# Performance work log

Hardware: AMD Instinct MI355X
Metric: run time of the kernel (lower is better)

Reference implementation:

```python
import jax, jax.numpy as jnp
import numpy as np

EPS = 1e-5
BN_GAMMA = 1.0
BN_BETA = 1e-4  # per torch init: BN weight=1, bias=0.0001


def bn(h):
    # BatchNorm1d in training mode: biased batch variance
    mu = h.mean(axis=0)
    var = h.var(axis=0)
    return (h - mu) * (BN_GAMMA / jnp.sqrt(var + EPS)) + BN_BETA


def gcn_conv(h, W, b, row, col, n, edge_weight=None):
    # PyG-style GCNConv: linear -> add self loops (w=1) -> sym deg norm -> scatter-sum
    h = h @ W
    e = row.shape[0]
    ew = jnp.ones((e,), h.dtype) if edge_weight is None else edge_weight
    loop = jnp.arange(n, dtype=row.dtype)
    r = jnp.concatenate([row, loop])
    c = jnp.concatenate([col, loop])
    w = jnp.concatenate([ew, jnp.ones((n,), h.dtype)])
    deg = jax.ops.segment_sum(w, r, num_segments=n)
    dinv = jnp.where(deg > 0, jax.lax.rsqrt(deg + jnp.where(deg > 0, 0.0, 1.0)), 0.0)
    norm = dinv[r] * w * dinv[c]  # [E+N]
    msg = h[r] * norm[:, None]    # gather + per-edge scale
    out = jax.ops.segment_sum(msg, c, num_segments=n)  # scatter-aggregate
    return out + b


def readout(h, W1, b1, W2, b2):
    h = bn(h) @ W1 + b1
    h = bn(jax.nn.relu(h)) @ W2 + b2
    return jax.nn.log_softmax(h, axis=-1)


def setup_inputs() -> dict:
    key = jax.random.key(0)
    ks = jax.random.split(key, 12)
    N, E, F, H, C = 50000, 800000, 128, 128, 10
    s = 0.05
    return {
        "x": jax.random.normal(ks[0], (N, F), jnp.float32),
        "edge_index": jax.random.randint(ks[1], (2, E), 0, N, jnp.int32),
        "perm": jax.random.permutation(ks[2], N).astype(jnp.int32),
        "W_feat": jax.random.normal(ks[3], (F, H), jnp.float32) * s,
        "b_feat": jnp.zeros((H,), jnp.float32),
        "W_convs": jax.random.normal(ks[4], (3, H, H), jnp.float32) * s,
        "b_convs": jnp.zeros((3, H), jnp.float32),
        "W_ea": jax.random.normal(ks[5], (2 * H, 2), jnp.float32) * s,
        "b_ea": jnp.zeros((2,), jnp.float32),
        "W_na": jax.random.normal(ks[6], (H, 2), jnp.float32) * s,
        "b_na": jnp.zeros((2,), jnp.float32),
        "W_ctx": jax.random.normal(ks[7], (H, H), jnp.float32) * s,
        "b_ctx": jnp.zeros((H,), jnp.float32),
        "W_obj": jax.random.normal(ks[8], (H, H), jnp.float32) * s,
        "b_obj": jnp.zeros((H,), jnp.float32),
        "W_fc1": jax.random.normal(ks[9], (3, H, H), jnp.float32) * s,  # c,o,co
        "b_fc1": jnp.zeros((3, H), jnp.float32),
        "W_fc2": jax.random.normal(ks[10], (3, H, C), jnp.float32) * s,
        "b_fc2": jnp.zeros((3, C), jnp.float32),
    }


def reference(x, edge_index, perm, W_feat, b_feat, W_convs, b_convs, W_ea, b_ea,
              W_na, b_na, W_ctx, b_ctx, W_obj, b_obj, W_fc1, b_fc1, W_fc2, b_fc2):
    n = x.shape[0]
    row, col = edge_index[0], edge_index[1]
    h = bn(x)
    h = jax.nn.relu(h @ W_feat + b_feat)  # conv_feat has gfn=True -> pure linear
    for i in range(3):
        h = jax.nn.relu(gcn_conv(bn(h), W_convs[i], b_convs[i], row, col, n))
    edge_rep = jnp.concatenate([h[row], h[col]], axis=-1)  # [E, 2H]
    edge_att = jax.nn.softmax(edge_rep @ W_ea + b_ea, axis=-1)
    node_att = jax.nn.softmax(h @ W_na + b_na, axis=-1)
    xc = node_att[:, 0:1] * h
    xo = node_att[:, 1:2] * h
    xc = jax.nn.relu(gcn_conv(bn(xc), W_ctx, b_ctx, row, col, n, edge_att[:, 0]))
    xo = jax.nn.relu(gcn_conv(bn(xo), W_obj, b_obj, row, col, n, edge_att[:, 1]))
    xc_logis = readout(xc, W_fc1[0], b_fc1[0], W_fc2[0], b_fc2[0])
    xo_logis = readout(xo, W_fc1[1], b_fc1[1], W_fc2[1], b_fc2[1])
    xco_logis = readout(xc[perm] + xo, W_fc1[2], b_fc1[2], W_fc2[2], b_fc2[2])
    return (xc_logis, xo_logis, xco_logis)
```

## Files before the change

kernel.cpp:

```cpp
#include <hip/hip_runtime.h>
#include <math.h>

#define H 128
#define NCLS 10
#define EPS 1e-5f
#define BN_BETA 1e-4f
#define CS_BLOCKS 256

typedef unsigned short u16;
typedef unsigned int u32;
typedef __attribute__((ext_vector_type(8))) short short8;
typedef __attribute__((ext_vector_type(4))) float floatx4;

__device__ inline float bflo(u32 u) { union { u32 i; float f; } a; a.i = u << 16; return a.f; }
__device__ inline float bfhi(u32 u) { union { u32 i; float f; } a; a.i = u & 0xffff0000u; return a.f; }
__device__ inline u16 f2bf(float f) {
  union { float f; u32 i; } v; v.f = f;
  return (u16)((v.i + 0x7fff + ((v.i >> 16) & 1)) >> 16);
}
__device__ inline u32 pack2(float a, float b) { return (u32)f2bf(a) | ((u32)f2bf(b) << 16); }

__device__ inline void reduce_partials(const float* __restrict__ P, int nb, int stride,
                                       int off0, int f, float* su_out, float* sq_out) {
  float su[8] = {0, 0, 0, 0, 0, 0, 0, 0}, sq[8] = {0, 0, 0, 0, 0, 0, 0, 0};
// ... 9 lines not shown
  for (; b < nb; b++) {
    const float* p = P + (size_t)b * stride + off0;
    su[0] += p[f];
    sq[0] += p[128 + f];
  }
  *su_out = ((su[0] + su[1]) + (su[2] + su[3])) + ((su[4] + su[5]) + (su[6] + su[7]));
  *sq_out = ((sq[0] + sq[1]) + (sq[2] + sq[3])) + ((sq[4] + sq[5]) + (sq[6] + sq[7]));
}

__device__ inline void fold256_body(const float* P, int nb, int stride, int off0,
                                    const float* W, const float* bias, float invN,
                                    int kp, u16* Wt, float* cf) {
  int f = threadIdx.x & 127;
  int half = threadIdx.x >> 7;
  int k = kp * 2 + half;
  float su, sq;
  reduce_partials(P, nb, stride, off0, f, &su, &sq);
  float mu = su * invN;
  float var = sq * invN - mu * mu;
  float s = 1.0f / sqrtf(fmaxf(var, 0.f) + EPS);
  float w = W[(size_t)f * H + k];
  Wt[(size_t)k * H + f] = f2bf(s * w);
  __shared__ float red[2][128];
  red[half][f] = (BN_BETA - mu * s) * w;
  __syncthreads();
  for (int o = 64; o > 0; o >>= 1) {
    if (f < o) red[half][f] += red[half][f + o];
    __syncthreads();
  }
  if (f == 0) cf[k] = red[half][0] + (bias ? bias[k] : 0.f);
}

__device__ inline void hist_body(const int* __restrict__ row, const int* __restrict__ col,
                                 int E, int* cnt, float* deg, int blk) {
  int e = blk * 256 + threadIdx.x;
  if (e < E) {
    atomicAdd(&cnt[col[e]], 1);
    atomicAdd(&deg[row[e]], 1.0f);
  }
}

__device__ inline void xstats_body(const float* __restrict__ x, int n4,
                                   float* __restrict__ stp, int blk) {
  int tid = threadIdx.x;
  int lane = tid & 63, wave = tid >> 6;
  float s[4] = {0, 0, 0, 0}, q[4] = {0, 0, 0, 0};
  int step = CS_BLOCKS * 256;
  for (int i = blk * 256 + tid; i < n4; i += step) {
    float4 v = ((const float4*)x)[i];
    s[0] += v.x; q[0] += v.x * v.x; s[1] += v.y; q[1] += v.y * v.y;
    s[2] += v.z; q[2] += v.z * v.z; s[3] += v.w; q[3] += v.w * v.w;
  }
#pragma unroll
  for (int k = 0; k < 4; k++) { s[k] += __shfl_xor(s[k], 32); q[k] += __shfl_xor(q[k], 32); }
  __shared__ float smx[4][256];
  int col = (lane & 31) * 4;
  if (lane < 32) {
#pragma unroll
    for (int k = 0; k < 4; k++) { smx[wave][col + k] = s[k]; smx[wave][128 + col + k] = q[k]; }
  }
  __syncthreads();
  stp[(size_t)blk * 256 + tid] = smx[0][tid] + smx[1][tid] + smx[2][tid] + smx[3][tid];
}

__device__ inline void scanA_body(const int* cnt, const float* deg, int N,
                                  int* partial, float* dinv, float* degc, int blk) {
  int i = blk * 256 + threadIdx.x;
  if (i < N) {
    dinv[i] = 1.0f / sqrtf(deg[i] + 1.0f);
    degc[i] = 0.f;
  }
  __shared__ int sdA[256];
  sdA[threadIdx.x] = (i < N) ? cnt[i] : 0;
  __syncthreads();
  for (int o = 128; o > 0; o >>= 1) {
    if (threadIdx.x < o) sdA[threadIdx.x] += sdA[threadIdx.x + o];
    __syncthreads();
  }
  if (threadIdx.x == 0) partial[blk] = sdA[0];
}

__device__ inline void scanB_body(const int* partial, int nb, int* blockoff) {
  __shared__ int sdB[256];
  int t = threadIdx.x;
  int v = (t < nb) ? partial[t] : 0;
  sdB[t] = v;
  __syncthreads();
  for (int o = 1; o < 256; o <<= 1) {
    int x = (t >= o) ? sdB[t - o] : 0;
    __syncthreads();
    sdB[t] += x;
    __syncthreads();
  }
  blockoff[t] = sdB[t] - v;
}

__device__ inline void scanC_body(const int* cnt, int N, const int* blockoff,
                                  int* off, int* cur, int E, int blk) {
  __shared__ int sdC[256];
  int t = threadIdx.x;
  int i = blk * 256 + t;
  int v = (i < N) ? cnt[i] : 0;
  sdC[t] = v;
  __syncthreads();
  for (int o = 1; o < 256; o <<= 1) {
    int x = (t >= o) ? sdC[t - o] : 0;
    __syncthreads();
    sdC[t] += x;
    __syncthreads();
  }
  if (i < N) {
    int ex = blockoff[blk] + sdC[t] - v;
    off[i] = ex;
    cur[i] = ex;
  }
  if (i == 0) off[N] = E;
}

__device__ inline void place_body(const int* row, const int* col, int E, int* cur,
                                  const float* dinv, int* csr_src, int* slot_of,
                                  float* wn, int blk) {
  int e = blk * 256 + threadIdx.x;
  if (e < E) {
    int r = row[e];
    int slot = atomicAdd(&cur[col[e]], 1);
    csr_src[slot] = r;
    slot_of[e] = slot;
    wn[slot] = dinv[r];
  }
}

__device__ inline void eatt_body(const int* row, const int* col, int E,
                                 const float2* p01, const float2* q01,
                                 const float* b_ea, const int* slot_of,
                                 float* att0s, float* degc, int blk) {
  int e = blk * 256 + threadIdx.x;
  if (e >= E) return;
  int r = row[e], c = col[e];
  float2 p = p01[r], q = q01[c];
  float l0 = p.x + q.x + b_ea[0];
  float l1 = p.y + q.y + b_ea[1];
  float a0 = 1.0f / (1.0f + expf(l1 - l0));
  att0s[slot_of[e]] = a0;
  atomicAdd(&degc[r], a0);
}

__device__ inline void xprestats_body(const u16* __restrict__ h,
                                      const float2* __restrict__ na01, int n4,
                                      float* __restrict__ stp, int blk) {
  int tid = threadIdx.x;
  int lane = tid & 63, wave = tid >> 6;
  float sc[4] = {0, 0, 0, 0}, qc[4] = {0, 0, 0, 0};
  float so[4] = {0, 0, 0, 0}, qo[4] = {0, 0, 0, 0};
  int step = CS_BLOCKS * 256;
  for (int i = blk * 256 + tid; i < n4; i += step) {
    int n = i >> 5;
    uint2 u = ((const uint2*)h)[i];
    float v0 = bflo(u.x), v1 = bfhi(u.x), v2 = bflo(u.y), v3 = bfhi(u.y);
    float2 ab = na01[n];
    float a = ab.x, b = ab.y;
    float c0 = v0 * a, c1 = v1 * a, c2 = v2 * a, c3 = v3 * a;
    float o0 = v0 * b, o1 = v1 * b, o2 = v2 * b, o3 = v3 * b;
    sc[0] += c0; qc[0] += c0 * c0; sc[1] += c1; qc[1] += c1 * c1;
    sc[2] += c2; qc[2] += c2 * c2; sc[3] += c3; qc[3] += c3 * c3;
    so[0] += o0; qo[0] += o0 * o0; so[1] += o1; qo[1] += o1 * o1;
    so[2] += o2; qo[2] += o2 * o2; so[3] += o3; qo[3] += o3 * o3;
  }
#pragma unroll
  for (int k = 0; k < 4; k++) {
    sc[k] += __shfl_xor(sc[k], 32); qc[k] += __shfl_xor(qc[k], 32);
    so[k] += __shfl_xor(so[k], 32); qo[k] += __shfl_xor(qo[k], 32);
  }
  __shared__ float smp[4][512];
  int col = (lane & 31) * 4;
  if (lane < 32) {
#pragma unroll
    for (int k = 0; k < 4; k++) {
      smp[wave][col + k] = sc[k];
      smp[wave][128 + col + k] = qc[k];
      smp[wave][256 + col + k] = so[k];
      smp[wave][384 + col + k] = qo[k];
    }
  }
  __syncthreads();
  float r0 = smp[0][tid] + smp[1][tid] + smp[2][tid] + smp[3][tid];
  float r1 = smp[0][256 + tid] + smp[1][256 + tid] + smp[2][256 + tid] + smp[3][256 + tid];
  stp[(size_t)blk * 512 + tid] = r0;
  stp[(size_t)blk * 512 + 256 + tid] = r1;
}

__device__ inline void wa2_body(const int* csr_src, const float* att0s,
                                const float* deg, const float* degc,
                                const float2* na01, float2* wfa, float2* wfr,
                                int E, int blk) {
  int i = blk * 256 + threadIdx.x;
  if (i >= E) return;
  int s = csr_src[i];
  float a0 = att0s[i];
  float2 na = na01[s];
  float dgc = degc[s];
  float r0 = a0 / sqrtf(dgc + 1.0f);
  float r1 = (1.0f - a0) / sqrtf(deg[s] - dgc + 1.0f);
  wfa[i] = make_float2(r0 * na.x, r1 * na.y);
  wfr[i] = make_float2(r0, r1);
}

__device__ inline void gemm_core(const u16* A, const float* Afp, const u16* Bt,
                                 const float* cf, const float* b2, const float* sumw,
                                 u16* C, int N, int relu, int blk, float* stp) {
  int tid = threadIdx.x;
  int wave = tid >> 6, lane = tid & 63;
  int l15 = lane & 15, quad = lane >> 4;
  int row0 = (blk * 4 + wave) * 16;
  if (row0 >= N && !stp) return;
  int arow = row0 + l15;
  short8 a[4];
  short8 z8 = {0, 0, 0, 0, 0, 0, 0, 0};
  if (Afp) {
#pragma unroll
    for (int k4 = 0; k4 < 4; k4++) {
      if (arow < N) {
        const float* p = Afp + (size_t)arow * H + k4 * 32 + quad * 8;
        float4 f0 = *(const float4*)p;
        float4 f1 = *(const float4*)(p + 4);
        union { short8 s8; u32 u[4]; } cv;
        cv.u[0] = pack2(f0.x, f0.y); cv.u[1] = pack2(f0.z, f0.w);
        cv.u[2] = pack2(f1.x, f1.y); cv.u[3] = pack2(f1.z, f1.w);
        a[k4] = cv.s8;
      } else a[k4] = z8;
    }
  } else {
#pragma unroll
    for (int k4 = 0; k4 < 4; k4++)
      a[k4] = (arow < N) ? *(const short8*)(A + (size_t)arow * H + k4 * 32 + quad * 8) : z8;
  }
  float srow[4];
  if (sumw) {
#pragma unroll
    for (int r = 0; r < 4; r++) {
// ... 18 lines not shown
#pragma unroll
    for (int r = 0; r < 4; r++) {
      int row = row0 + quad * 4 + r;
      if (row < N) {
        float v = acc[r] + (sumw ? srow[r] * base + bb : base);
        if (relu) v = fmaxf(v, 0.f);
        s_ += v; q_ += v * v;
        C[(size_t)row * H + col] = f2bf(v);
      }
    }
    ps[nt] = s_; pq[nt] = q_;
  }
  if (stp) {
    __shared__ float sred[4][256];
#pragma unroll
    for (int nt = 0; nt < 8; nt++) {
      ps[nt] += __shfl_xor(ps[nt], 16); ps[nt] += __shfl_xor(ps[nt], 32);
      pq[nt] += __shfl_xor(pq[nt], 16); pq[nt] += __shfl_xor(pq[nt], 32);
    }
    if (quad == 0) {
#pragma unroll
      for (int nt = 0; nt < 8; nt++) {
        sred[wave][nt * 16 + l15] = ps[nt];
        sred[wave][128 + nt * 16 + l15] = pq[nt];
      }
    }
    __syncthreads();
    stp[(size_t)blk * 256 + tid] =
        sred[0][tid] + sred[1][tid] + sred[2][tid] + sred[3][tid];
  }
}

__global__ __launch_bounds__(256) void hist_xstats_kernel(
    const int* row, const int* col, int E, int* cnt, float* deg, int gE,
    const float* x, int n4, float* stpX) {
  if ((int)blockIdx.x < gE) hist_body(row, col, E, cnt, deg, blockIdx.x);
  else xstats_body(x, n4, stpX, blockIdx.x - gE);
}

__global__ __launch_bounds__(256) void scanA_fold_kernel(
    const int* cnt, const float* deg, int N, int* partial, float* dinv, float* degc,
    int SB, const float* stpX, const float* W_feat, const float* b_feat, float invN,
    u16* WtA, float* cfA) {
  if ((int)blockIdx.x < SB) scanA_body(cnt, deg, N, partial, dinv, degc, blockIdx.x);
  else fold256_body(stpX, CS_BLOCKS, 256, 0, W_feat, b_feat, invN, blockIdx.x - SB, WtA, cfA);
}

__global__ __launch_bounds__(256) void scanB_gemmx_kernel(
    const int* partial, int nb, int* blockoff,
    const float* x, const u16* WtA, const float* cfA, u16* C, int N, float* stpG) {
  if (blockIdx.x == 0) scanB_body(partial, nb, blockoff);
  else gemm_core(nullptr, x, WtA, cfA, nullptr, nullptr, C, N, 1, blockIdx.x - 1, stpG);
}

__global__ __launch_bounds__(256) void scanC_fold_kernel(
    const int* cnt, int N, const int* blockoff, int* off, int* cur, int E, int SB,
    const float* stpG, int nbG, const float* Wc, float invN, u16* WtB, float* cfB) {
  if ((int)blockIdx.x < SB) scanC_body(cnt, N, blockoff, off, cur, E, blockIdx.x);
  else fold256_body(stpG, nbG, 256, 0, Wc, nullptr, invN, blockIdx.x - SB, WtB, cfB);
}

__global__ __launch_bounds__(256) void place_gemm_kernel(
    const int* row, const int* col, int E, int* cur, const float* dinv,
    int* csr_src, int* slot_of, float* wn, int gE,
    const u16* A, const u16* WtB, const float* cfB, u16* C, int N) {
  if ((int)blockIdx.x < gE)
    place_body(row, col, E, cur, dinv, csr_src, slot_of, wn, blockIdx.x);
  else
    gemm_core(A, nullptr, WtB, cfB, nullptr, nullptr, C, N, 0, blockIdx.x - gE, nullptr);
}

__global__ __launch_bounds__(256) void eatt_xpre_kernel(
    const int* row, const int* col, int E, const float2* p01, const float2* q01,
    const float* b_ea, const int* slot_of, float* att0s, float* degc, int gE,
    const u16* h, const float2* na01, int n4, float* stpPre) {
  if ((int)blockIdx.x < gE)
    eatt_body(row, col, E, p01, q01, b_ea, slot_of, att0s, degc, blockIdx.x);
  else
    xprestats_body(h, na01, n4, stpPre, blockIdx.x - gE);
}

__global__ __launch_bounds__(256) void wa2_fold2_kernel(
    const int* csr_src, const float* att0s, const float* deg, const float* degc,
    const float2* na01, float2* wfa, float2* wfr, int E, int gE,
    const float* stpPre, const float* W_ctx, const float* W_obj, float invN,
    u16* Wt2, float* cf2) {
  if ((int)blockIdx.x < gE)
    wa2_body(csr_src, att0s, deg, degc, na01, wfa, wfr, E, blockIdx.x);
  else {
    int b = blockIdx.x - gE;
    int j = b >> 6, kp = b & 63;
    fold256_body(stpPre, CS_BLOCKS, 512, j * 256, j ? W_obj : W_ctx, nullptr, invN, kp,
                 Wt2 + (size_t)j * H * H, cf2 + j * H);
  }
}

__global__ __launch_bounds__(256) void fold256_kernel(
    const float* P, int nb, const float* W, const float* bias, float invN,
    u16* Wt, float* cf) {
  fold256_body(P, nb, 256, 0, W, bias, invN, blockIdx.x, Wt, cf);
}

__global__ __launch_bounds__(256) void fold3_kernel(
    const float* PC, int nbC, const float* PO, int nbO, const float* PCO, int nbCO,
    const float* W_fc1, const float* b_fc1, float invN, u16* Wt3, float* cf3) {
  int j = blockIdx.x / 64, kp = blockIdx.x % 64;
  const float* P = (j == 0) ? PC : (j == 1) ? PO : PCO;
  int nb = (j == 0) ? nbC : (j == 1) ? nbO : nbCO;
  fold256_body(P, nb, 256, 0, W_fc1 + (size_t)j * H * H, b_fc1 + j * H, invN, kp,
               Wt3 + (size_t)j * H * H, cf3 + j * H);
}

__global__ __launch_bounds__(128) void fold10x3_kernel(
    const float* stpZ, int nb, const float* W_fc2, const float* b_fc2, float invN,
    float* W2f, float* c2f) {
  int j = blockIdx.x / NCLS, k = blockIdx.x % NCLS;
  const float* P = stpZ + (size_t)j * nb * 256;
  int f = threadIdx.x;
  float su, sq;
  reduce_partials(P, nb, 256, 0, f, &su, &sq);
  float mu = su * invN;
  float var = sq * invN - mu * mu;
  float s = 1.0f / sqrtf(fmaxf(var, 0.f) + EPS);
  float w = W_fc2[(size_t)j * H * NCLS + (size_t)f * NCLS + k];
  W2f[(size_t)j * H * NCLS + (size_t)f * NCLS + k] = s * w;
  __shared__ float red1[H];
  red1[f] = (BN_BETA - mu * s) * w;
  __syncthreads();
  for (int o = 64; o > 0; o >>= 1) {
    if (f < o) red1[f] += red1[f + o];
    __syncthreads();
  }
  if (f == 0) c2f[j * 16 + k] = red1[0] + b_fc2[j * NCLS + k];
}

__global__ __launch_bounds__(256) void gemm_kernel(
    const u16* A, const u16* Bt, const float* cf, u16* C, int N, int relu) {
  gemm_core(A, nullptr, Bt, cf, nullptr, nullptr, C, N, relu, blockIdx.x, nullptr);
}

__global__ __launch_bounds__(256) void gemm2sw_kernel(
    u16* B0, u16* B1, const u16* Wt2, const float* cf2,
    const float* b0, const float* b1, const float* sw0, const float* sw1,
// ... 72 lines not shown
    int ix[8]; float wv[8];
#pragma unroll
    for (int u = 0; u < 8; u++) {
      int e = s + g + u * 4;
      bool ok = e < s1;
      int e2 = ok ? e : s0;
      ix[u] = csr_src[e2];
      wv[u] = ok ? wseg[e2] : 0.f;
    }
    uint4 uu[8];
#pragma unroll
    for (int u = 0; u < 8; u++) uu[u] = T[(size_t)ix[u] * 16 + li];
#pragma unroll
    for (int u = 0; u < 8; u++) { float w = wv[u] * dv; ACC8(acc, uu[u], w) }
  }
#pragma unroll
  for (int j = 0; j < 8; j++) {
    acc[j] += __shfl_xor(acc[j], 16);
    acc[j] += __shfl_xor(acc[j], 32);
  }
  if (g == 0) {
    float o[8];
#pragma unroll
    for (int j = 0; j < 8; j++) o[j] = fmaxf(acc[j] + bias[li * 8 + j], 0.f);
    uint4 w4;
    w4.x = pack2(o[0], o[1]); w4.y = pack2(o[2], o[3]);
    w4.z = pack2(o[4], o[5]); w4.w = pack2(o[6], o[7]);
    ((uint4*)out)[(size_t)v * 16 + li] = w4;
  }
}

__global__ __launch_bounds__(256) void aggdual_kernel(
    const u16* __restrict__ h, const int* __restrict__ csr_src,
    const float2* __restrict__ wfa, const float2* __restrict__ wfr,
    const int* __restrict__ off, const float* __restrict__ deg,
    const float* __restrict__ degc, const float2* __restrict__ na01,
    u16* __restrict__ gc, u16* __restrict__ go,
    float* __restrict__ sumw_c, float* __restrict__ sumw_o, int N) {
  int v = blockIdx.x * 4 + (threadIdx.x >> 6);
  if (v >= N) return;
  int lane = threadIdx.x & 63;
  int g = lane >> 4, li = lane & 15;
  const uint4* T = (const uint4*)h;
  float dgc = degc[v];
  float dvc = 1.0f / sqrtf(dgc + 1.0f);
  float dvo = 1.0f / sqrtf(deg[v] - dgc + 1.0f);
  float ac[8] = {0.f, 0.f, 0.f, 0.f, 0.f, 0.f, 0.f, 0.f};
  float ao[8] = {0.f, 0.f, 0.f, 0.f, 0.f, 0.f, 0.f, 0.f};
  float swc = 0.f, swo = 0.f;
  if (g == 0) {
    uint4 u = T[(size_t)v * 16 + li];
    float2 na = na01[v];
    float wc = dvc * dvc, wo = dvo * dvo;
    float wch = wc * na.x, woh = wo * na.y;
    ACC8(ac, u, wch)
    ACC8(ao, u, woh)
  }
  int s0 = off[v], s1 = off[v + 1];
  for (int s = s0; s < s1; s += 16) {
    int ix[4]; float2 fa[4], fr[4];
#pragma unroll
    for (int u = 0; u < 4; u++) {
      int e = s + g + u * 4;
      bool ok = e < s1;
      int e2 = ok ? e : s0;
      ix[u] = csr_src[e2];
      fa[u] = ok ? wfa[e2] : make_float2(0.f, 0.f);
      fr[u] = ok ? wfr[e2] : make_float2(0.f, 0.f);
    }
    uint4 uu[4];
#pragma unroll
    for (int u = 0; u < 4; u++) uu[u] = T[(size_t)ix[u] * 16 + li];
#pragma unroll
    for (int u = 0; u < 4; u++) {
      float wc = fa[u].x * dvc; ACC8(ac, uu[u], wc)
      float wo = fa[u].y * dvo; ACC8(ao, uu[u], wo)
      swc += fr[u].x; swo += fr[u].y;
    }
  }
#pragma unroll
  for (int j = 0; j < 8; j++) {
    ac[j] += __shfl_xor(ac[j], 16); ac[j] += __shfl_xor(ac[j], 32);
    ao[j] += __shfl_xor(ao[j], 16); ao[j] += __shfl_xor(ao[j], 32);
  }
  swc += __shfl_xor(swc, 16); swc += __shfl_xor(swc, 32);
  swo += __shfl_xor(swo, 16); swo += __shfl_xor(swo, 32);
  if (g == 0) {
    uint4 wc4, wo4;
    wc4.x = pack2(ac[0], ac[1]); wc4.y = pack2(ac[2], ac[3]);
    wc4.z = pack2(ac[4], ac[5]); wc4.w = pack2(ac[6], ac[7]);
    wo4.x = pack2(ao[0], ao[1]); wo4.y = pack2(ao[2], ao[3]);
    wo4.z = pack2(ao[4], ao[5]); wo4.w = pack2(ao[6], ao[7]);
    ((uint4*)gc)[(size_t)v * 16 + li] = wc4;
    ((uint4*)go)[(size_t)v * 16 + li] = wo4;
    if (li == 0) {
      sumw_c[v] = dvc * swc + dvc * dvc;
      sumw_o[v] = dvo * swo + dvo * dvo;
    }
  }
}

__global__ __launch_bounds__(256) void natt_kernel(
    const u16* __restrict__ h, int N,
    const float* __restrict__ W_na, const float* __restrict__ b_na,
    const float* __restrict__ W_ea,
    float2* __restrict__ na01, float2* __restrict__ p01, float2* __restrict__ q01) {
  int n = blockIdx.x * 256 + threadIdx.x;
  if (n >= N) return;
  float sa0 = 0, sa1 = 0, sp0 = 0, sp1 = 0, sq0 = 0, sq1 = 0;
  const uint2* hr = (const uint2*)(h + (size_t)n * H);
  for (int c = 0; c < 32; c++) {
    uint2 u = hr[c];
    float v0 = bflo(u.x), v1 = bfhi(u.x), v2 = bflo(u.y), v3 = bfhi(u.y);
    int k = c * 4;
    sa0 += v0 * W_na[k * 2] + v1 * W_na[k * 2 + 2] + v2 * W_na[k * 2 + 4] + v3 * W_na[k * 2 + 6];
    sa1 += v0 * W_na[k * 2 + 1] + v1 * W_na[k * 2 + 3] + v2 * W_na[k * 2 + 5] + v3 * W_na[k * 2 + 7];
    sp0 += v0 * W_ea[k * 2] + v1 * W_ea[k * 2 + 2] + v2 * W_ea[k * 2 + 4] + v3 * W_ea[k * 2 + 6];
    sp1 += v0 * W_ea[k * 2 + 1] + v1 * W_ea[k * 2 + 3] + v2 * W_ea[k * 2 + 5] + v3 * W_ea[k * 2 + 7];
    sq0 += v0 * W_ea[(H + k) * 2] + v1 * W_ea[(H + k) * 2 + 2] + v2 * W_ea[(H + k) * 2 + 4] + v3 * W_ea[(H + k) * 2 + 6];
    sq1 += v0 * W_ea[(H + k) * 2 + 1] + v1 * W_ea[(H + k) * 2 + 3] + v2 * W_ea[(H + k) * 2 + 5] + v3 * W_ea[(H + k) * 2 + 7];
  }
  sa0 += b_na[0]; sa1 += b_na[1];
  float m = fmaxf(sa0, sa1);
  float e0 = expf(sa0 - m), e1 = expf(sa1 - m);
  float inv = 1.f / (e0 + e1);
  na01[n] = make_float2(e0 * inv, e1 * inv);
  p01[n] = make_float2(sp0, sp1);
  q01[n] = make_float2(sq0, sq1);
}

__global__ __launch_bounds__(256) void permadd_stats_kernel(
    const u16* __restrict__ xc, const u16* __restrict__ xo,
    const int* __restrict__ perm, u16* __restrict__ out, int n4, float* __restrict__ stp) {
  int tid = threadIdx.x;
  int lane = tid & 63, wave = tid >> 6;
  float s[4] = {0, 0, 0, 0}, q[4] = {0, 0, 0, 0};
  int step = CS_BLOCKS * 256;
  for (int i = blockIdx.x * 256 + tid; i < n4; i += step) {
    int n = i >> 5, k = i & 31;
    int p = perm[n];
    uint2 a = ((const uint2*)xc)[(size_t)p * 32 + k];
    uint2 b = ((const uint2*)xo)[i];
    float f0 = bflo(a.x) + bflo(b.x), f1 = bfhi(a.x) + bfhi(b.x);
    float f2 = bflo(a.y) + bflo(b.y), f3 = bfhi(a.y) + bfhi(b.y);
    ((uint2*)out)[i] = make_uint2(pack2(f0, f1), pack2(f2, f3));
    s[0] += f0; q[0] += f0 * f0; s[1] += f1; q[1] += f1 * f1;
    s[2] += f2; q[2] += f2 * f2; s[3] += f3; q[3] += f3 * f3;
  }
#pragma unroll
  for (int k = 0; k < 4; k++) { s[k] += __shfl_xor(s[k], 32); q[k] += __shfl_xor(q[k], 32); }
  __shared__ float smq[4][256];
  int col = (lane & 31) * 4;
  if (lane < 32) {
#pragma unroll
    for (int k = 0; k < 4; k++) { smq[wave][col + k] = s[k]; smq[wave][128 + col + k] = q[k]; }
  }
  __syncthreads();
  stp[(size_t)blockIdx.x * 256 + tid] = smq[0][tid] + smq[1][tid] + smq[2][tid] + smq[3][tid];
}

__global__ __launch_bounds__(256) void fc2x3_kernel(
    const u16* __restrict__ z0, const u16* __restrict__ z1, const u16* __restrict__ z2,
    const float* __restrict__ W2f, const float* __restrict__ c2f,
    float* __restrict__ outp, int N, int gN) {
  int j = blockIdx.x / gN, blk = blockIdx.x % gN;
  int n = blk * 256 + threadIdx.x;
  if (n >= N) return;
  const u16* z = (j == 0) ? z0 : (j == 1) ? z1 : z2;
  const float* W2 = W2f + (size_t)j * H * NCLS;
  const float* c2 = c2f + j * 16;
  float* op = outp + (size_t)j * N * NCLS;
  float acc[NCLS];
#pragma unroll
  for (int c = 0; c < NCLS; c++) acc[c] = c2[c];
  const uint2* zr = (const uint2*)(z + (size_t)n * H);
  for (int c4 = 0; c4 < 32; c4++) {
    uint2 u = zr[c4];
    float v[4] = {bflo(u.x), bfhi(u.x), bflo(u.y), bfhi(u.y)};
    int k = c4 * 4;
#pragma unroll
    for (int jj = 0; jj < 4; jj++)
#pragma unroll
      for (int c = 0; c < NCLS; c++) acc[c] += v[jj] * W2[(k + jj) * NCLS + c];
  }
  float m = acc[0];
#pragma unroll
  for (int c = 1; c < NCLS; c++) m = fmaxf(m, acc[c]);
  float s = 0.f;
#pragma unroll
  for (int c = 0; c < NCLS; c++) s += expf(acc[c] - m);
  float lse = logf(s) + m;
// ... 19 lines not shown
  const float* b_ea = (const float*)d_in[8];
  const float* W_na = (const float*)d_in[9];
  const float* b_na = (const float*)d_in[10];
  const float* W_ctx = (const float*)d_in[11];
  const float* b_ctx = (const float*)d_in[12];
  const float* W_obj = (const float*)d_in[13];
  const float* b_obj = (const float*)d_in[14];
  const float* W_fc1 = (const float*)d_in[15];
  const float* b_fc1 = (const float*)d_in[16];
  const float* W_fc2 = (const float*)d_in[17];
  const float* b_fc2 = (const float*)d_in[18];
  float* out = (float*)d_out;

  const int gG = (N + 63) / 64;
  const int gN = (N + 255) / 256;
  const int gE = (E + 255) / 256;
  const int SB = (N + 255) / 256;
  const int n4 = N * 32;
  const int gAgg = (N + 3) / 4;
  const float invN = 1.0f / (float)N;

  char* base = (char*)d_ws;
  size_t off_b = 0;
  auto alloc = [&](size_t bytes) -> void* {
    void* p = base + off_b;
    off_b = (off_b + bytes + 255) & ~(size_t)255;
    return p;
  };
  size_t NB2 = (size_t)N * H * sizeof(u16);
  u16* bufA = (u16*)alloc(NB2);
  u16* bufB = (u16*)alloc(NB2);
  u16* bufC = (u16*)alloc(NB2);
  u16* bufD = (u16*)alloc(NB2);
  int* cnt = (int*)alloc(2 * (size_t)N * 4);
  float* deg = (float*)(cnt + N);
  float* degc = (float*)alloc((size_t)N * 4);
  float* stpX = (float*)alloc((size_t)CS_BLOCKS * 256 * 4);
  float* stpG = (float*)alloc(3 * (size_t)gG * 256 * 4);
  float* stpPre = (float*)alloc((size_t)CS_BLOCKS * 512 * 4);
  float* stpCO = (float*)alloc((size_t)CS_BLOCKS * 256 * 4);
  int* off = (int*)alloc(((size_t)N + 1) * 4);
  int* cur = (int*)alloc((size_t)N * 4);
  float* dinv = (float*)alloc((size_t)N * 4);
  float* sumw_c = (float*)alloc((size_t)N * 4);
  float* sumw_o = (float*)alloc((size_t)N * 4);
  float2* na01 = (float2*)alloc((size_t)N * 8);
  float2* p01 = (float2*)alloc((size_t)N * 8);
  float2* q01 = (float2*)alloc((size_t)N * 8);
  int* partial = (int*)alloc(256 * 4);
  int* blockoff = (int*)alloc(256 * 4);
  u16* WtA = (u16*)alloc((size_t)H * H * 2);
  u16* WtB = (u16*)alloc((size_t)H * H * 2);
  u16* Wt2 = (u16*)alloc(2 * (size_t)H * H * 2);
  u16* Wt3 = (u16*)alloc(3 * (size_t)H * H * 2);
  float* cfA = (float*)alloc(H * 4);
  float* cfB = (float*)alloc(H * 4);
  float* cf2 = (float*)alloc(2 * H * 4);
  float* cf3 = (float*)alloc(3 * H * 4);
  float* W2f = (float*)alloc(3 * (size_t)H * NCLS * 4);
  float* c2f = (float*)alloc(3 * 16 * 4);
  int* csr_src = (int*)alloc((size_t)E * 4);
  int* slot_of = (int*)alloc((size_t)E * 4);
  float* att0s = (float*)alloc((size_t)E * 4);
  float* wn = (float*)alloc((size_t)E * 4);
  float2* wfa = (float2*)alloc((size_t)E * 8);
  float2* wfr = (float2*)alloc((size_t)E * 8);

  hipMemsetAsync(cnt, 0, 2 * (size_t)N * 4, stream);

  hist_xstats_kernel<<<gE + CS_BLOCKS, 256, 0, stream>>>(row, col, E, cnt, deg, gE,
                                                         x, n4, stpX);
  scanA_fold_kernel<<<SB + 64, 256, 0, stream>>>(cnt, deg, N, partial, dinv, degc, SB,
                                                 stpX, W_feat, b_feat, invN, WtA, cfA);
  scanB_gemmx_kernel<<<1 + gG, 256, 0, stream>>>(partial, SB, blockoff, x, WtA, cfA,
                                                 bufA, N, stpG);
  scanC_fold_kernel<<<SB + 64, 256, 0, stream>>>(cnt, N, blockoff, off, cur, E, SB,
                                                 stpG, gG, W_convs, invN, WtB, cfB);
  place_gemm_kernel<<<gE + gG, 256, 0, stream>>>(row, col, E, cur, dinv, csr_src,
                                                 slot_of, wn, gE, bufA, WtB, cfB,
                                                 bufB, N);
  agg_kernel<<<gAgg, 256, 0, stream>>>(bufB, csr_src, wn, off, dinv, b_convs, bufA, N);

  for (int i = 1; i < 3; ++i) {
    colstats_kernel<<<CS_BLOCKS, 256, 0, stream>>>(bufA, N, stpX);
    fold256_kernel<<<64, 256, 0, stream>>>(stpX, CS_BLOCKS, W_convs + (size_t)i * H * H,
                                           nullptr, invN, WtB, cfB);
    gemm_kernel<<<gG, 256, 0, stream>>>(bufA, WtB, cfB, bufB, N, 0);
    agg_kernel<<<gAgg, 256, 0, stream>>>(bufB, csr_src, wn, off, dinv,
                                         b_convs + (size_t)i * H, bufA, N);
  }

  natt_kernel<<<gN, 256, 0, stream>>>(bufA, N, W_na, b_na, W_ea, na01, p01, q01);
  eatt_xpre_kernel<<<gE + CS_BLOCKS, 256, 0, stream>>>(row, col, E, p01, q01, b_ea,
                                                       slot_of, att0s, degc, gE,
                                                       bufA, na01, n4, stpPre);
  wa2_fold2_kernel<<<gE + 128, 256, 0, stream>>>(csr_src, att0s, deg, degc, na01,
                                                 wfa, wfr, E, gE, stpPre, W_ctx,
                                                 W_obj, invN, Wt2, cf2);
  aggdual_kernel<<<gAgg, 256, 0, stream>>>(bufA, csr_src, wfa, wfr, off, deg, degc,
                                           na01, bufC, bufD, sumw_c, sumw_o, N);
  gemm2sw_kernel<<<2 * gG, 256, 0, stream>>>(bufC, bufD, Wt2, cf2, b_ctx, b_obj,
                                             sumw_c, sumw_o, N, gG, stpG);

  permadd_stats_kernel<<<CS_BLOCKS, 256, 0, stream>>>(bufC, bufD, perm, bufA, n4, stpCO);

  fold3_kernel<<<192, 256, 0, stream>>>(stpG, gG, stpG + (size_t)gG * 256, gG,
                                        stpCO, CS_BLOCKS, W_fc1, b_fc1, invN, Wt3, cf3);
  gemm3_kernel<<<3 * gG, 256, 0, stream>>>(bufC, bufD, bufA, Wt3, cf3, N, gG, stpG);
  fold10x3_kernel<<<3 * NCLS, 128, 0, stream>>>(stpG, gG, W_fc2, b_fc2, invN, W2f, c2f);
  fc2x3_kernel<<<3 * gN, 256, 0, stream>>>(bufC, bufD, bufA, W2f, c2f, out, N, gN);
}
```

Before: 904.5 us.

## Replace scatter atomics with rank-based CSR placement and segmented degree sums

The histogram pass now records each edge's atomic rank for both in- and out-degree. CSR placement then computes slots deterministically from offsets plus rank, with no second atomic pass. The float atomicAdd for attention-weighted degrees is replaced by writing into an out-CSR order and summing per node. The wa2 per-edge weight precompute is folded into aggdual, which recomputes weights from att0s, cnt_out and degc gathered per source. Part of the fc1 fold is fused into the permadd kernel. This cuts atomic contention and E-sized intermediates, at the cost of extra rank arrays, a second scan, and more random gathers inside the aggregation loop.

```diff
diff --git a/kernel.cpp b/kernel.cpp
--- a/kernel.cpp
+++ b/kernel.cpp
@@ -65,11 +65,12 @@
 }
 
 __device__ inline void hist_body(const int* __restrict__ row, const int* __restrict__ col,
-                                 int E, int* cnt, float* deg, int blk) {
+                                 int E, int* cnt_in, int* cnt_out,
+                                 int* rank_in, int* rank_out, int blk) {
   int e = blk * 256 + threadIdx.x;
   if (e < E) {
-    atomicAdd(&cnt[col[e]], 1);
-    atomicAdd(&deg[row[e]], 1.0f);
+    rank_in[e] = atomicAdd(&cnt_in[col[e]], 1);
+    rank_out[e] = atomicAdd(&cnt_out[row[e]], 1);
   }
 }
 
@@ -96,24 +97,30 @@
   stp[(size_t)blk * 256 + tid] = smx[0][tid] + smx[1][tid] + smx[2][tid] + smx[3][tid];
 }
 
-__device__ inline void scanA_body(const int* cnt, const float* deg, int N,
-                                  int* partial, float* dinv, float* degc, int blk) {
+__device__ inline void scanA_body(const int* cnt_in, const int* cnt_out, int N,
+                                  int* partial_in, int* partial_out, float* dinv, int blk) {
   int i = blk * 256 + threadIdx.x;
-  if (i < N) {
-    dinv[i] = 1.0f / sqrtf(deg[i] + 1.0f);
-    degc[i] = 0.f;
-  }
+  int vo = (i < N) ? cnt_out[i] : 0;
+  if (i < N) dinv[i] = 1.0f / sqrtf((float)vo + 1.0f);
   __shared__ int sdA[256];
-  sdA[threadIdx.x] = (i < N) ? cnt[i] : 0;
+  sdA[threadIdx.x] = (i < N) ? cnt_in[i] : 0;
   __syncthreads();
   for (int o = 128; o > 0; o >>= 1) {
     if (threadIdx.x < o) sdA[threadIdx.x] += sdA[threadIdx.x + o];
     __syncthreads();
   }
-  if (threadIdx.x == 0) partial[blk] = sdA[0];
-}
-
-__device__ inline void scanB_body(const int* partial, int nb, int* blockoff) {
+  if (threadIdx.x == 0) partial_in[blk] = sdA[0];
+  __syncthreads();
+  sdA[threadIdx.x] = vo;
+  __syncthreads();
+  for (int o = 128; o > 0; o >>= 1) {
+    if (threadIdx.x < o) sdA[threadIdx.x] += sdA[threadIdx.x + o];
+    __syncthreads();
+  }
+  if (threadIdx.x == 0) partial_out[blk] = sdA[0];
+}
+
+__device__ inline void scanB1(const int* partial, int nb, int* blockoff) {
   __shared__ int sdB[256];
   int t = threadIdx.x;
   int v = (t < nb) ? partial[t] : 0;
@@ -126,10 +133,11 @@
     __syncthreads();
   }
   blockoff[t] = sdB[t] - v;
-}
-
-__device__ inline void scanC_body(const int* cnt, int N, const int* blockoff,
-                                  int* off, int* cur, int E, int blk) {
+  __syncthreads();
+}
+
+__device__ inline void scanC1(const int* cnt, int N, const int* blockoff,
+                              int* off, int E, int blk) {
   __shared__ int sdC[256];
   int t = threadIdx.x;
   int i = blk * 256 + t;
@@ -142,31 +150,31 @@
     sdC[t] += x;
     __syncthreads();
   }
-  if (i < N) {
-    int ex = blockoff[blk] + sdC[t] - v;
-    off[i] = ex;
-    cur[i] = ex;
-  }
+  if (i < N) off[i] = blockoff[blk] + sdC[t] - v;
   if (i == 0) off[N] = E;
-}
-
-__device__ inline void place_body(const int* row, const int* col, int E, int* cur,
-                                  const float* dinv, int* csr_src, int* slot_of,
-                                  float* wn, int blk) {
+  __syncthreads();
+}
+
+__device__ inline void place_body(const int* row, const int* col, int E,
+                                  const int* rank_in, const int* rank_out,
+                                  const int* off_in, const int* off_out,
+                                  const float* dinv, int* csr_src, int* slot_in,
+                                  int* sout, float* wn, int blk) {
   int e = blk * 256 + threadIdx.x;
   if (e < E) {
-    int r = row[e];
-    int slot = atomicAdd(&cur[col[e]], 1);
-    csr_src[slot] = r;
-    slot_of[e] = slot;
-    wn[slot] = dinv[r];
+    int c = col[e], r = row[e];
+    int si = off_in[c] + rank_in[e];
+    csr_src[si] = r;
+    slot_in[e] = si;
+    wn[si] = dinv[r];
+    sout[e] = off_out[r] + rank_out[e];
   }
 }
 
 __device__ inline void eatt_body(const int* row, const int* col, int E,
                                  const float2* p01, const float2* q01,
-                                 const float* b_ea, const int* slot_of,
-                                 float* att0s, float* degc, int blk) {
+                                 const float* b_ea, const int* slot_in,
+                                 const int* sout, float* att0s, float* att_r, int blk) {
   int e = blk * 256 + threadIdx.x;
   if (e >= E) return;
   int r = row[e], c = col[e];
@@ -174,8 +182,18 @@
   float l0 = p.x + q.x + b_ea[0];
   float l1 = p.y + q.y + b_ea[1];
   float a0 = 1.0f / (1.0f + expf(l1 - l0));
-  att0s[slot_of[e]] = a0;
-  atomicAdd(&degc[r], a0);
+  att0s[slot_in[e]] = a0;
+  att_r[sout[e]] = a0;
+}
+
+__device__ inline void degsum_body(const float* att_r, const int* off_out,
+                                   float* degc, int N, int blk) {
+  int v = blk * 256 + threadIdx.x;
+  if (v >= N) return;
+  int s0 = off_out[v], s1 = off_out[v + 1];
+  float s = 0.f;
+  for (int i = s0; i < s1; i++) s += att_r[i];
+  degc[v] = s;
 }
 
 __device__ inline void xprestats_body(const u16* __restrict__ h,
@@ -222,22 +240,6 @@
   stp[(size_t)blk * 512 + 256 + tid] = r1;
 }
 
-__device__ inline void wa2_body(const int* csr_src, const float* att0s,
-                                const float* deg, const float* degc,
-                                const float2* na01, float2* wfa, float2* wfr,
-                                int E, int blk) {
-  int i = blk * 256 + threadIdx.x;
-  if (i >= E) return;
-  int s = csr_src[i];
-  float a0 = att0s[i];
-  float2 na = na01[s];
-  float dgc = degc[s];
-  float r0 = a0 / sqrtf(dgc + 1.0f);
-  float r1 = (1.0f - a0) / sqrtf(deg[s] - dgc + 1.0f);
-  wfa[i] = make_float2(r0 * na.x, r1 * na.y);
-  wfr[i] = make_float2(r0, r1);
-}
-
 __device__ inline void gemm_core(const u16* A, const float* Afp, const u16* Bt,
                                  const float* cf, const float* b2, const float* sumw,
                                  u16* C, int N, int relu, int blk, float* stp) {
@@ -322,83 +324,127 @@
 }
 
 __global__ __launch_bounds__(256) void hist_xstats_kernel(
-    const int* row, const int* col, int E, int* cnt, float* deg, int gE,
-    const float* x, int n4, float* stpX) {
-  if ((int)blockIdx.x < gE) hist_body(row, col, E, cnt, deg, blockIdx.x);
-  else xstats_body(x, n4, stpX, blockIdx.x - gE);
+    const int* row, const int* col, int E, int* cnt_in, int* cnt_out,
+    int* rank_in, int* rank_out, int gE, const float* x, int n4, float* stpX) {
+  if ((int)blockIdx.x < gE)
+    hist_body(row, col, E, cnt_in, cnt_out, rank_in, rank_out, blockIdx.x);
+  else
+    xstats_body(x, n4, stpX, blockIdx.x - gE);
 }
 
 __global__ __launch_bounds__(256) void scanA_fold_kernel(
-    const int* cnt, const float* deg, int N, int* partial, float* dinv, float* degc,
-    int SB, const float* stpX, const float* W_feat, const float* b_feat, float invN,
-    u16* WtA, float* cfA) {
-  if ((int)blockIdx.x < SB) scanA_body(cnt, deg, N, partial, dinv, degc, blockIdx.x);
-  else fold256_body(stpX, CS_BLOCKS, 256, 0, W_feat, b_feat, invN, blockIdx.x - SB, WtA, cfA);
+    const int* cnt_in, const int* cnt_out, int N, int* partial_in, int* partial_out,
+    float* dinv, int SB, const float* stpX, const float* W_feat, const float* b_feat,
+    float invN, u16* WtA, float* cfA) {
+  if ((int)blockIdx.x < SB)
+    scanA_body(cnt_in, cnt_out, N, partial_in, partial_out, dinv, blockIdx.x);
+  else
+    fold256_body(stpX, CS_BLOCKS, 256, 0, W_feat, b_feat, invN, blockIdx.x - SB, WtA, cfA);
 }
 
 __global__ __launch_bounds__(256) void scanB_gemmx_kernel(
-    const int* partial, int nb, int* blockoff,
-    const float* x, const u16* WtA, const float* cfA, u16* C, int N, float* stpG) {
-  if (blockIdx.x == 0) scanB_body(partial, nb, blockoff);
-  else gemm_core(nullptr, x, WtA, cfA, nullptr, nullptr, C, N, 1, blockIdx.x - 1, stpG);
+    const int* partial_in, const int* partial_out, int nb, int* blockoff_in,
+    int* blockoff_out, const float* x, const u16* WtA, const float* cfA, u16* C,
+    int N, float* stpG) {
+  if (blockIdx.x == 0) {
+    scanB1(partial_in, nb, blockoff_in);
+    scanB1(partial_out, nb, blockoff_out);
+  } else {
+    gemm_core(nullptr, x, WtA, cfA, nullptr, nullptr, C, N, 1, blockIdx.x - 1, stpG);
+  }
 }
 
 __global__ __launch_bounds__(256) void scanC_fold_kernel(
-    const int* cnt, int N, const int* blockoff, int* off, int* cur, int E, int SB,
+    const int* cnt_in, const int* cnt_out, int N, const int* blockoff_in,
+    const int* blockoff_out, int* off_in, int* off_out, int E, int SB,
     const float* stpG, int nbG, const float* Wc, float invN, u16* WtB, float* cfB) {
-  if ((int)blockIdx.x < SB) scanC_body(cnt, N, blockoff, off, cur, E, blockIdx.x);
-  else fold256_body(stpG, nbG, 256, 0, Wc, nullptr, invN, blockIdx.x - SB, WtB, cfB);
+  if ((int)blockIdx.x < SB) {
+    scanC1(cnt_in, N, blockoff_in, off_in, E, blockIdx.x);
+    scanC1(cnt_out, N, blockoff_out, off_out, E, blockIdx.x);
+  } else {
+    fold256_body(stpG, nbG, 256, 0, Wc, nullptr, invN, blockIdx.x - SB, WtB, cfB);
+  }
 }
 
 __global__ __launch_bounds__(256) void place_gemm_kernel(
-    const int* row, const int* col, int E, int* cur, const float* dinv,
-    int* csr_src, int* slot_of, float* wn, int gE,
+    const int* row, const int* col, int E, const int* rank_in, const int* rank_out,
+    const int* off_in, const int* off_out, const float* dinv, int* csr_src,
+    int* slot_in, int* sout, float* wn, int gE,
     const u16* A, const u16* WtB, const float* cfB, u16* C, int N) {
   if ((int)blockIdx.x < gE)
-    place_body(row, col, E, cur, dinv, csr_src, slot_of, wn, blockIdx.x);
+    place_body(row, col, E, rank_in, rank_out, off_in, off_out, dinv, csr_src,
+               slot_in, sout, wn, blockIdx.x);
   else
     gemm_core(A, nullptr, WtB, cfB, nullptr, nullptr, C, N, 0, blockIdx.x - gE, nullptr);
 }
 
 __global__ __launch_bounds__(256) void eatt_xpre_kernel(
     const int* row, const int* col, int E, const float2* p01, const float2* q01,
-    const float* b_ea, const int* slot_of, float* att0s, float* degc, int gE,
-    const u16* h, const float2* na01, int n4, float* stpPre) {
+    const float* b_ea, const int* slot_in, const int* sout, float* att0s,
+    float* att_r, int gE, const u16* h, const float2* na01, int n4, float* stpPre) {
   if ((int)blockIdx.x < gE)
-    eatt_body(row, col, E, p01, q01, b_ea, slot_of, att0s, degc, blockIdx.x);
+    eatt_body(row, col, E, p01, q01, b_ea, slot_in, sout, att0s, att_r, blockIdx.x);
   else
     xprestats_body(h, na01, n4, stpPre, blockIdx.x - gE);
 }
 
-__global__ __launch_bounds__(256) void wa2_fold2_kernel(
-    const int* csr_src, const float* att0s, const float* deg, const float* degc,
-    const float2* na01, float2* wfa, float2* wfr, int E, int gE,
+__global__ __launch_bounds__(256) void degsum_fold2_kernel(
+    const float* att_r, const int* off_out, float* degc, int N, int gN,
     const float* stpPre, const float* W_ctx, const float* W_obj, float invN,
     u16* Wt2, float* cf2) {
-  if ((int)blockIdx.x < gE)
-    wa2_body(csr_src, att0s, deg, degc, na01, wfa, wfr, E, blockIdx.x);
+  if ((int)blockIdx.x < gN)
+    degsum_body(att_r, off_out, degc, N, blockIdx.x);
   else {
-    int b = blockIdx.x - gE;
+    int b = blockIdx.x - gN;
     int j = b >> 6, kp = b & 63;
     fold256_body(stpPre, CS_BLOCKS, 512, j * 256, j ? W_obj : W_ctx, nullptr, invN, kp,
                  Wt2 + (size_t)j * H * H, cf2 + j * H);
   }
+}
+
+__global__ __launch_bounds__(256) void permadd_fold31_kernel(
+    const u16* xc, const u16* xo, const int* perm, u16* outb, int n4, float* stpCO,
+    const float* stpG, int nbG, const float* W_fc1, const float* b_fc1, float invN,
+    u16* Wt3, float* cf3) {
+  int tid = threadIdx.x;
+  if ((int)blockIdx.x >= CS_BLOCKS) {
+    int b = blockIdx.x - CS_BLOCKS;
+    int j = b >> 6, kp = b & 63;
+    fold256_body(stpG + (size_t)j * nbG * 256, nbG, 256, 0, W_fc1 + (size_t)j * H * H,
+                 b_fc1 + j * H, invN, kp, Wt3 + (size_t)j * H * H, cf3 + j * H);
+    return;
+  }
+  int blk = blockIdx.x;
+  int lane = tid & 63, wave = tid >> 6;
+  float s[4] = {0, 0, 0, 0}, q[4] = {0, 0, 0, 0};
+  int step = CS_BLOCKS * 256;
+  for (int i = blk * 256 + tid; i < n4; i += step) {
+    int n = i >> 5, k = i & 31;
+    int p = perm[n];
+    uint2 a = ((const uint2*)xc)[(size_t)p * 32 + k];
+    uint2 b = ((const uint2*)xo)[i];
+    float f0 = bflo(a.x) + bflo(b.x), f1 = bfhi(a.x) + bfhi(b.x);
+    float f2 = bflo(a.y) + bflo(b.y), f3 = bfhi(a.y) + bfhi(b.y);
+    ((uint2*)outb)[i] = make_uint2(pack2(f0, f1), pack2(f2, f3));
+    s[0] += f0; q[0] += f0 * f0; s[1] += f1; q[1] += f1 * f1;
+    s[2] += f2; q[2] += f2 * f2; s[3] += f3; q[3] += f3 * f3;
+  }
+#pragma unroll
+  for (int k = 0; k < 4; k++) { s[k] += __shfl_xor(s[k], 32); q[k] += __shfl_xor(q[k], 32); }
+  __shared__ float smq[4][256];
+  int col = (lane & 31) * 4;
+  if (lane < 32) {
+#pragma unroll
+    for (int k = 0; k < 4; k++) { smq[wave][col + k] = s[k]; smq[wave][128 + col + k] = q[k]; }
+  }
+  __syncthreads();
+  stpCO[(size_t)blk * 256 + tid] = smq[0][tid] + smq[1][tid] + smq[2][tid] + smq[3][tid];
 }
 
 __global__ __launch_bounds__(256) void fold256_kernel(
     const float* P, int nb, const float* W, const float* bias, float invN,
     u16* Wt, float* cf) {
   fold256_body(P, nb, 256, 0, W, bias, invN, blockIdx.x, Wt, cf);
-}
-
-__global__ __launch_bounds__(256) void fold3_kernel(
-    const float* PC, int nbC, const float* PO, int nbO, const float* PCO, int nbCO,
-    const float* W_fc1, const float* b_fc1, float invN, u16* Wt3, float* cf3) {
-  int j = blockIdx.x / 64, kp = blockIdx.x % 64;
-  const float* P = (j == 0) ? PC : (j == 1) ? PO : PCO;
-  int nb = (j == 0) ? nbC : (j == 1) ? nbO : nbCO;
-  fold256_body(P, nb, 256, 0, W_fc1 + (size_t)j * H * H, b_fc1 + j * H, invN, kp,
-               Wt3 + (size_t)j * H * H, cf3 + j * H);
 }
 
 __global__ __launch_bounds__(128) void fold10x3_kernel(
@@ -537,9 +583,9 @@
 
 __global__ __launch_bounds__(256) void aggdual_kernel(
     const u16* __restrict__ h, const int* __restrict__ csr_src,
-    const float2* __restrict__ wfa, const float2* __restrict__ wfr,
-    const int* __restrict__ off, const float* __restrict__ deg,
+    const float* __restrict__ att0s, const int* __restrict__ cnt_out,
     const float* __restrict__ degc, const float2* __restrict__ na01,
+    const int* __restrict__ off,
     u16* __restrict__ gc, u16* __restrict__ go,
     float* __restrict__ sumw_c, float* __restrict__ sumw_o, int N) {
   int v = blockIdx.x * 4 + (threadIdx.x >> 6);
@@ -549,7 +595,7 @@
   const uint4* T = (const uint4*)h;
   float dgc = degc[v];
   float dvc = 1.0f / sqrtf(dgc + 1.0f);
-  float dvo = 1.0f / sqrtf(deg[v] - dgc + 1.0f);
+  float dvo = 1.0f / sqrtf((float)cnt_out[v] - dgc + 1.0f);
   float ac[8] = {0.f, 0.f, 0.f, 0.f, 0.f, 0.f, 0.f, 0.f};
   float ao[8] = {0.f, 0.f, 0.f, 0.f, 0.f, 0.f, 0.f, 0.f};
   float swc = 0.f, swo = 0.f;
@@ -563,24 +609,36 @@
   }
   int s0 = off[v], s1 = off[v + 1];
   for (int s = s0; s < s1; s += 16) {
-    int ix[4]; float2 fa[4], fr[4];
+    int ix[4]; float a0v[4];
 #pragma unroll
     for (int u = 0; u < 4; u++) {
       int e = s + g + u * 4;
       bool ok = e < s1;
       int e2 = ok ? e : s0;
       ix[u] = csr_src[e2];
-      fa[u] = ok ? wfa[e2] : make_float2(0.f, 0.f);
-      fr[u] = ok ? wfr[e2] : make_float2(0.f, 0.f);
+      a0v[u] = ok ? att0s[e2] : 0.f;
+      if (!ok) a0v[u] = -1.f;
     }
     uint4 uu[4];
-#pragma unroll
-    for (int u = 0; u < 4; u++) uu[u] = T[(size_t)ix[u] * 16 + li];
+    float2 nav[4];
+    float dS[4], dC[4];
 #pragma unroll
     for (int u = 0; u < 4; u++) {
-      float wc = fa[u].x * dvc; ACC8(ac, uu[u], wc)
-      float wo = fa[u].y * dvo; ACC8(ao, uu[u], wo)
-      swc += fr[u].x; swo += fr[u].y;
+      int sidx = ix[u];
+      uu[u] = T[(size_t)sidx * 16 + li];
+      nav[u] = na01[sidx];
+      dS[u] = (float)cnt_out[sidx];
+      dC[u] = degc[sidx];
+    }
+#pragma unroll
+    for (int u = 0; u < 4; u++) {
+      float a0 = a0v[u];
+      bool ok = a0 >= 0.f;
+      float r0 = ok ? a0 / sqrtf(dC[u] + 1.0f) : 0.f;
+      float r1 = ok ? (1.0f - a0) / sqrtf(dS[u] - dC[u] + 1.0f) : 0.f;
+      float wc = r0 * nav[u].x * dvc; ACC8(ac, uu[u], wc)
+      float wo = r1 * nav[u].y * dvo; ACC8(ao, uu[u], wo)
+      swc += r0; swo += r1;
     }
   }
 #pragma unroll
@@ -632,36 +690,6 @@
   na01[n] = make_float2(e0 * inv, e1 * inv);
   p01[n] = make_float2(sp0, sp1);
   q01[n] = make_float2(sq0, sq1);
-}
-
-__global__ __launch_bounds__(256) void permadd_stats_kernel(
-    const u16* __restrict__ xc, const u16* __restrict__ xo,
-    const int* __restrict__ perm, u16* __restrict__ out, int n4, float* __restrict__ stp) {
-  int tid = threadIdx.x;
-  int lane = tid & 63, wave = tid >> 6;
-  float s[4] = {0, 0, 0, 0}, q[4] = {0, 0, 0, 0};
-  int step = CS_BLOCKS * 256;
-  for (int i = blockIdx.x * 256 + tid; i < n4; i += step) {
-    int n = i >> 5, k = i & 31;
-    int p = perm[n];
-    uint2 a = ((const uint2*)xc)[(size_t)p * 32 + k];
-    uint2 b = ((const uint2*)xo)[i];
-    float f0 = bflo(a.x) + bflo(b.x), f1 = bfhi(a.x) + bfhi(b.x);
-    float f2 = bflo(a.y) + bflo(b.y), f3 = bfhi(a.y) + bfhi(b.y);
-    ((uint2*)out)[i] = make_uint2(pack2(f0, f1), pack2(f2, f3));
-    s[0] += f0; q[0] += f0 * f0; s[1] += f1; q[1] += f1 * f1;
-    s[2] += f2; q[2] += f2 * f2; s[3] += f3; q[3] += f3 * f3;
-  }
-#pragma unroll
-  for (int k = 0; k < 4; k++) { s[k] += __shfl_xor(s[k], 32); q[k] += __shfl_xor(q[k], 32); }
-  __shared__ float smq[4][256];
-  int col = (lane & 31) * 4;
-  if (lane < 32) {
-#pragma unroll
-    for (int k = 0; k < 4; k++) { smq[wave][col + k] = s[k]; smq[wave][128 + col + k] = q[k]; }
-  }
-  __syncthreads();
-  stp[(size_t)blockIdx.x * 256 + tid] = smq[0][tid] + smq[1][tid] + smq[2][tid] + smq[3][tid];
 }
 
 __global__ __launch_bounds__(256) void fc2x3_kernel(
@@ -747,23 +775,25 @@
   u16* bufB = (u16*)alloc(NB2);
   u16* bufC = (u16*)alloc(NB2);
   u16* bufD = (u16*)alloc(NB2);
-  int* cnt = (int*)alloc(2 * (size_t)N * 4);
-  float* deg = (float*)(cnt + N);
+  int* cnt_in = (int*)alloc(2 * (size_t)N * 4);
+  int* cnt_out = cnt_in + N;
   float* degc = (float*)alloc((size_t)N * 4);
   float* stpX = (float*)alloc((size_t)CS_BLOCKS * 256 * 4);
   float* stpG = (float*)alloc(3 * (size_t)gG * 256 * 4);
   float* stpPre = (float*)alloc((size_t)CS_BLOCKS * 512 * 4);
   float* stpCO = (float*)alloc((size_t)CS_BLOCKS * 256 * 4);
-  int* off = (int*)alloc(((size_t)N + 1) * 4);
-  int* cur = (int*)alloc((size_t)N * 4);
+  int* off_in = (int*)alloc(((size_t)N + 1) * 4);
+  int* off_out = (int*)alloc(((size_t)N + 1) * 4);
   float* dinv = (float*)alloc((size_t)N * 4);
   float* sumw_c = (float*)alloc((size_t)N * 4);
   float* sumw_o = (float*)alloc((size_t)N * 4);
   float2* na01 = (float2*)alloc((size_t)N * 8);
   float2* p01 = (float2*)alloc((size_t)N * 8);
   float2* q01 = (float2*)alloc((size_t)N * 8);
-  int* partial = (int*)alloc(256 * 4);
-  int* blockoff = (int*)alloc(256 * 4);
+  int* partial_in = (int*)alloc(256 * 4);
+  int* partial_out = (int*)alloc(256 * 4);
+  int* blockoff_in = (int*)alloc(256 * 4);
+  int* blockoff_out = (int*)alloc(256 * 4);
   u16* WtA = (u16*)alloc((size_t)H * H * 2);
   u16* WtB = (u16*)alloc((size_t)H * H * 2);
   u16* Wt2 = (u16*)alloc(2 * (size_t)H * H * 2);
@@ -774,53 +804,57 @@
   float* cf3 = (float*)alloc(3 * H * 4);
   float* W2f = (float*)alloc(3 * (size_t)H * NCLS * 4);
   float* c2f = (float*)alloc(3 * 16 * 4);
+  int* rank_in = (int*)alloc((size_t)E * 4);
+  int* rank_out = (int*)alloc((size_t)E * 4);
   int* csr_src = (int*)alloc((size_t)E * 4);
-  int* slot_of = (int*)alloc((size_t)E * 4);
+  int* slot_in = (int*)alloc((size_t)E * 4);
+  int* sout = (int*)alloc((size_t)E * 4);
   float* att0s = (float*)alloc((size_t)E * 4);
+  float* att_r = (float*)alloc((size_t)E * 4);
   float* wn = (float*)alloc((size_t)E * 4);
-  float2* wfa = (float2*)alloc((size_t)E * 8);
-  float2* wfr = (float2*)alloc((size_t)E * 8);
-
-  hipMemsetAsync(cnt, 0, 2 * (size_t)N * 4, stream);
-
-  hist_xstats_kernel<<<gE + CS_BLOCKS, 256, 0, stream>>>(row, col, E, cnt, deg, gE,
-                                                         x, n4, stpX);
-  scanA_fold_kernel<<<SB + 64, 256, 0, stream>>>(cnt, deg, N, partial, dinv, degc, SB,
-                                                 stpX, W_feat, b_feat, invN, WtA, cfA);
-  scanB_gemmx_kernel<<<1 + gG, 256, 0, stream>>>(partial, SB, blockoff, x, WtA, cfA,
-                                                 bufA, N, stpG);
-  scanC_fold_kernel<<<SB + 64, 256, 0, stream>>>(cnt, N, blockoff, off, cur, E, SB,
-                                                 stpG, gG, W_convs, invN, WtB, cfB);
-  place_gemm_kernel<<<gE + gG, 256, 0, stream>>>(row, col, E, cur, dinv, csr_src,
-                                                 slot_of, wn, gE, bufA, WtB, cfB,
-                                                 bufB, N);
-  agg_kernel<<<gAgg, 256, 0, stream>>>(bufB, csr_src, wn, off, dinv, b_convs, bufA, N);
+
+  hipMemsetAsync(cnt_in, 0, 2 * (size_t)N * 4, stream);
+
+  hist_xstats_kernel<<<gE + CS_BLOCKS, 256, 0, stream>>>(
+      row, col, E, cnt_in, cnt_out, rank_in, rank_out, gE, x, n4, stpX);
+  scanA_fold_kernel<<<SB + 64, 256, 0, stream>>>(
+      cnt_in, cnt_out, N, partial_in, partial_out, dinv, SB, stpX, W_feat, b_feat,
+      invN, WtA, cfA);
+  scanB_gemmx_kernel<<<1 + gG, 256, 0, stream>>>(
+      partial_in, partial_out, SB, blockoff_in, blockoff_out, x, WtA, cfA, bufA, N, stpG);
+  scanC_fold_kernel<<<SB + 64, 256, 0, stream>>>(
+      cnt_in, cnt_out, N, blockoff_in, blockoff_out, off_in, off_out, E, SB,
+      stpG, gG, W_convs, invN, WtB, cfB);
+  place_gemm_kernel<<<gE + gG, 256, 0, stream>>>(
+      row, col, E, rank_in, rank_out, off_in, off_out, dinv, csr_src, slot_in, sout,
+      wn, gE, bufA, WtB, cfB, bufB, N);
+  agg_kernel<<<gAgg, 256, 0, stream>>>(bufB, csr_src, wn, off_in, dinv, b_convs, bufA, N);
 
   for (int i = 1; i < 3; ++i) {
     colstats_kernel<<<CS_BLOCKS, 256, 0, stream>>>(bufA, N, stpX);
     fold256_kernel<<<64, 256, 0, stream>>>(stpX, CS_BLOCKS, W_convs + (size_t)i * H * H,
                                            nullptr, invN, WtB, cfB);
     gemm_kernel<<<gG, 256, 0, stream>>>(bufA, WtB, cfB, bufB, N, 0);
-    agg_kernel<<<gAgg, 256, 0, stream>>>(bufB, csr_src, wn, off, dinv,
+    agg_kernel<<<gAgg, 256, 0, stream>>>(bufB, csr_src, wn, off_in, dinv,
                                          b_convs + (size_t)i * H, bufA, N);
   }
 
   natt_kernel<<<gN, 256, 0, stream>>>(bufA, N, W_na, b_na, W_ea, na01, p01, q01);
-  eatt_xpre_kernel<<<gE + CS_BLOCKS, 256, 0, stream>>>(row, col, E, p01, q01, b_ea,
-                                                       slot_of, att0s, degc, gE,
-                                                       bufA, na01, n4, stpPre);
-  wa2_fold2_kernel<<<gE + 128, 256, 0, stream>>>(csr_src, att0s, deg, degc, na01,
-                                                 wfa, wfr, E, gE, stpPre, W_ctx,
-                                                 W_obj, invN, Wt2, cf2);
-  aggdual_kernel<<<gAgg, 256, 0, stream>>>(bufA, csr_src, wfa, wfr, off, deg, degc,
-                                           na01, bufC, bufD, sumw_c, sumw_o, N);
+  eatt_xpre_kernel<<<gE + CS_BLOCKS, 256, 0, stream>>>(
+      row, col, E, p01, q01, b_ea, slot_in, sout, att0s, att_r, gE,
+      bufA, na01, n4, stpPre);
+  degsum_fold2_kernel<<<gN + 128, 256, 0, stream>>>(
+      att_r, off_out, degc, N, gN, stpPre, W_ctx, W_obj, invN, Wt2, cf2);
+  aggdual_kernel<<<gAgg, 256, 0, stream>>>(bufA, csr_src, att0s, cnt_out, degc, na01,
+                                           off_in, bufC, bufD, sumw_c, sumw_o, N);
   gemm2sw_kernel<<<2 * gG, 256, 0, stream>>>(bufC, bufD, Wt2, cf2, b_ctx, b_obj,
                                              sumw_c, sumw_o, N, gG, stpG);
 
-  permadd_stats_kernel<<<CS_BLOCKS, 256, 0, stream>>>(bufC, bufD, perm, bufA, n4, stpCO);
-
-  fold3_kernel<<<192, 256, 0, stream>>>(stpG, gG, stpG + (size_t)gG * 256, gG,
-                                        stpCO, CS_BLOCKS, W_fc1, b_fc1, invN, Wt3, cf3);
+  permadd_fold31_kernel<<<CS_BLOCKS + 128, 256, 0, stream>>>(
+      bufC, bufD, perm, bufA, n4, stpCO, stpG, gG, W_fc1, b_fc1, invN, Wt3, cf3);
+  fold256_kernel<<<64, 256, 0, stream>>>(stpCO, CS_BLOCKS, W_fc1 + 2 * (size_t)H * H,
+                                         b_fc1 + 2 * H, invN, Wt3 + 2 * (size_t)H * H,
+                                         cf3 + 2 * H);
   gemm3_kernel<<<3 * gG, 256, 0, stream>>>(bufC, bufD, bufA, Wt3, cf3, N, gG, stpG);
   fold10x3_kernel<<<3 * NCLS, 128, 0, stream>>>(stpG, gG, W_fc2, b_fc2, invN, W2f, c2f);
   fc2x3_kernel<<<3 * gN, 256, 0, stream>>>(bufC, bufD, bufA, W2f, c2f, out, N, gN);
```

Result: faster. 833.7 us (-7.8%).
